# Kernel tuning notes

Hardware: AMD Instinct MI355X
Metric: run time of the kernel (lower is better)

The kernel has to match this reference:

```python
import jax, jax.numpy as jnp
import numpy as np

B, T, C = 4, 2048, 1024
N_HEAD = 16
HEAD_DIM = C // N_HEAD


def setup_inputs() -> dict:
    key = jax.random.key(0)
    k1, k2, k3 = jax.random.split(key, 3)
    x = jax.random.normal(k1, (B, T, C), dtype=jnp.float32)
    w_attn = jax.random.normal(k2, (C, 3 * C), dtype=jnp.float32) * 0.02
    b_attn = jnp.zeros((3 * C,), dtype=jnp.float32)
    # c_proj init stddev = 0.02 / sqrt(2 * n_layer), n_layer = 24
    w_proj = jax.random.normal(k3, (C, C), dtype=jnp.float32) * (0.02 / np.sqrt(48.0))
    b_proj = jnp.zeros((C,), dtype=jnp.float32)
    return {"x": x, "w_attn": w_attn, "b_attn": b_attn,
            "w_proj": w_proj, "b_proj": b_proj}


def reference(x, w_attn, b_attn, w_proj, b_proj):
    Bx, Tx, Cx = x.shape
    scale = 1.0 / jnp.sqrt(jnp.asarray(HEAD_DIM, dtype=x.dtype))
    qkv = x @ w_attn + b_attn                      # [B,T,3C]
    qkv = qkv.reshape(Bx, Tx, 3, N_HEAD, HEAD_DIM)
    q, k, v = qkv[:, :, 0], qkv[:, :, 1], qkv[:, :, 2]  # each [B,T,H,D]
    att = jnp.einsum('bthd,bThd->bhtT', q, k) * scale   # [B,H,T,T]
    mask = jnp.tril(jnp.ones((Tx, Tx), dtype=x.dtype)).reshape(1, 1, Tx, Tx)
    att = att * mask - 1e10 * (1 - mask)
    att = jax.nn.softmax(att, axis=-1)
    y = jnp.einsum('bhtT,bThd->bthd', att, v)      # [B,T,H,D]
    y = y.reshape(Bx, Tx, Cx)
    return y @ w_proj + b_proj
```

## Files before the change

### kernel.cpp

```cpp
#include <hip/hip_runtime.h>
#include <hip/hip_bf16.h>


typedef __attribute__((ext_vector_type(8)))  __bf16 bf16x8;
typedef __attribute__((ext_vector_type(4)))  float  f32x4;
typedef __attribute__((ext_vector_type(16))) float  f32x16;
typedef __attribute__((ext_vector_type(4)))  unsigned int u32x4;

#define AS1C(p) ((const __attribute__((address_space(1))) unsigned int*)(p))
#define AS3(p)  ((__attribute__((address_space(3))) unsigned int*)(p))

__device__ __forceinline__ unsigned short f2bfu(float f){
  __hip_bfloat16 h = __float2bfloat16(f);
  return __builtin_bit_cast(unsigned short, h);
}

__device__ __forceinline__ void plswapu(unsigned int &a, unsigned int &b){
  asm("v_permlane32_swap_b32 %0, %1" : "+v"(a), "+v"(b));
}
__device__ __forceinline__ unsigned int cvtpk(float lo, float hi){
  unsigned int r;
  asm("v_cvt_pk_bf16_f32 %0, %1, %2" : "=v"(r) : "v"(lo), "v"(hi));
  return r;
}
__device__ __forceinline__ float max3f(float a, float b, float c){
  float r;
  asm("v_max3_f32 %0, %1, %2, %3" : "=v"(r) : "v"(a), "v"(b), "v"(c));
  return r;
}


__global__ __launch_bounds__(256)
void f32_to_bf16_vec(const float* __restrict__ in, __hip_bfloat16* __restrict__ out, int n4){
  int stride = gridDim.x * blockDim.x;
  for (int i = blockIdx.x*blockDim.x + threadIdx.x; i < n4; i += stride){
    float4 v = reinterpret_cast<const float4*>(in)[i];
    ushort4 u;
    u.x = f2bfu(v.x); u.y = f2bfu(v.y); u.z = f2bfu(v.z); u.w = f2bfu(v.w);
    reinterpret_cast<ushort4*>(out)[i] = u;
  }
}

__global__ __launch_bounds__(256)
void transpose_to_bf16(const float* __restrict__ in, __hip_bfloat16* __restrict__ out, int R, int C){
  __shared__ float tile[32][33];
  const int tx = threadIdx.x & 31, ty = threadIdx.x >> 5;
  const int c0 = blockIdx.x*32, r0 = blockIdx.y*32;
  for (int i = ty; i < 32; i += 8)
    tile[i][tx] = in[(size_t)(r0+i)*C + c0 + tx];
  __syncthreads();
  for (int i = ty; i < 32; i += 8)
    out[(size_t)(c0+i)*R + r0 + tx] = __float2bfloat16(tile[tx][i]);
}


#define QSCALE 0.1803368801111244f

__device__ __forceinline__ void stage_ab(const __hip_bfloat16* __restrict__ A,
                                         const __hip_bfloat16* __restrict__ Bt,
                                         int m0, int n0, int K, int kt,
                                         __hip_bfloat16* sA, __hip_bfloat16* sB,
                                         int w, int l)
{
  const int k0 = kt*32;
  #pragma unroll
  for (int qq = 0; qq < 2; ++qq){
    const int c = qq*256 + w*64 + l;
    const int row = c>>2, kc = c&3;
    __builtin_amdgcn_global_load_lds(AS1C(A  + (size_t)(m0+row)*K + k0 + 8*kc),
                                     AS3(sA + (qq*256 + w*64)*8), 16, 0, 0);
    __builtin_amdgcn_global_load_lds(AS1C(Bt + (size_t)(n0+row)*K + k0 + 8*kc),
                                     AS3(sB + (qq*256 + w*64)*8), 16, 0, 0);
  }
}

template<int EPI>
__global__ __launch_bounds__(256)
void gemm_bf16(const __hip_bfloat16* __restrict__ A,
               const __hip_bfloat16* __restrict__ Bt,
               const float* __restrict__ bias,
               int M, int N, int K,
               __hip_bfloat16* __restrict__ q_s,
               __hip_bfloat16* __restrict__ k_s,
               __hip_bfloat16* __restrict__ vT_s,
               float* __restrict__ outf)
{
  __shared__ __align__(16) __hip_bfloat16 sA[2][128*32];
  __shared__ __align__(16) __hip_bfloat16 sB[2][128*32];
  const int tid = threadIdx.x, w = tid>>6, l = tid&63, g = l>>4, li = l&15;
  const int wm = w>>1, wn = w&1;

  const int nwg = gridDim.x, cpx = nwg >> 3;
  const int swz = (blockIdx.x & 7)*cpx + (blockIdx.x >> 3);
  const int nbx = N >> 7;
  const int m0 = (swz / nbx)*128, n0 = (swz % nbx)*128;

  f32x4 acc[4][4] = {};

  const int NT = K >> 5;
  stage_ab(A, Bt, m0, n0, K, 0, sA[0], sB[0], w, l);
  int cur = 0;

  for (int kt = 0; kt < NT; ++kt){
    __syncthreads();
    if (kt + 1 < NT)
      stage_ab(A, Bt, m0, n0, K, kt+1, sA[cur^1], sB[cur^1], w, l);

    bf16x8 af[4], bfr[4];
    #pragma unroll
    for (int mi = 0; mi < 4; ++mi)
      af[mi] = *reinterpret_cast<const bf16x8*>(sA[cur] + (wm*64 + mi*16 + li)*32 + 8*g);
    #pragma unroll
    for (int ni = 0; ni < 4; ++ni)
      bfr[ni] = *reinterpret_cast<const bf16x8*>(sB[cur] + (wn*64 + ni*16 + li)*32 + 8*g);
    #pragma unroll
    for (int mi = 0; mi < 4; ++mi)
      #pragma unroll
      for (int ni = 0; ni < 4; ++ni)
        acc[mi][ni] = __builtin_amdgcn_mfma_f32_16x16x32_bf16(af[mi], bfr[ni], acc[mi][ni], 0, 0, 0);
    cur ^= 1;
  }

  #pragma unroll
  for (int ni = 0; ni < 4; ++ni){
    const int col = n0 + wn*64 + ni*16 + li;
    const float bv = bias[col];
    #pragma unroll
    for (int mi = 0; mi < 4; ++mi){
      #pragma unroll
      for (int e = 0; e < 4; ++e){
        const int row = m0 + wm*64 + mi*16 + 4*g + e;
        const float val = acc[mi][ni][e] + bv;
        if (EPI == 0){
          const int three = col >> 10, h = (col >> 6) & 15, d = col & 63;
          const int b = row >> 11, t = row & 2047;
          const int bh = b*16 + h;
          if (three == 0)      q_s[((size_t)bh*2048 + t)*64 + d]  = __float2bfloat16(val*QSCALE);
          else if (three == 1) k_s[((size_t)bh*2048 + t)*64 + d]  = __float2bfloat16(val);
          else                 vT_s[((size_t)bh*64 + d)*2048 + t] = __float2bfloat16(val);
        } else {
          outf[(size_t)row*N + col] = val;
        }
      }
    }
  }
}


__device__ __forceinline__ void stage_kv64(const __hip_bfloat16* __restrict__ k_s,
                                           const __hip_bfloat16* __restrict__ vT_s,
                                           size_t base, int j,
                                           __hip_bfloat16* sk, __hip_bfloat16* svt,
                                           int tid)
{
  #pragma unroll
  for (int it = 0; it < 4; ++it){
    const int c = it*128 + tid;
    const int r = c>>3, cc = c&7;
    __builtin_amdgcn_global_load_lds(AS1C(k_s  + base + (size_t)(j*64 + r)*64 + 8*(cc ^ (r&7))),
                                     AS3(sk  + c*8), 16, 0, 0);
    __builtin_amdgcn_global_load_lds(AS1C(vT_s + base + (size_t)r*2048 + j*64 + 8*(cc ^ (r&7))),
                                     AS3(svt + c*8), 16, 0, 0);
  }
}

__device__ __forceinline__ bf16x8 ldtile(const __hip_bfloat16* t, int row, int chunk){
  return *reinterpret_cast<const bf16x8*>(t + row*64 + ((chunk ^ (row&7))*8));
}

__global__ __launch_bounds__(128, 3)
void flash_attn(const __hip_bfloat16* __restrict__ q_s,
                const __hip_bfloat16* __restrict__ k_s,
                const __hip_bfloat16* __restrict__ vT_s,
                __hip_bfloat16* __restrict__ y_s)
{
  __shared__ __align__(16) __hip_bfloat16 sk [2][64*64];
  __shared__ __align__(16) __hip_bfloat16 svt[2][64*64];

  const int tid = threadIdx.x, w = tid>>6, l = tid&63;
  const int lq = l&31, hf = l>>5, h4 = 4*hf;
  const int bid = blockIdx.x;
  const int xcd = bid & 7, sl = (bid>>3) & 7;
  const int v = 31 - (bid >> 6);
  const int bh = xcd*8 + sl;
  const size_t base = (size_t)bh * (2048*64);
  const int b = bh >> 4, hh = bh & 15;

  const int tw = 2*v + w;
  const int jd = v;
  const int qabs = 32*tw + lq;
  const int rel = 32*w + lq;

  bf16x8 qf[4];
  #pragma unroll
  for (int ks = 0; ks < 4; ++ks)
    qf[ks] = *reinterpret_cast<const bf16x8*>(q_s + base + (size_t)qabs*64 + 16*ks + 8*hf);

  f32x16 o0 = {}, o1 = {};
  float mrun = -1e30f, lrun = 0.f;

  stage_kv64(k_s, vT_s, base, 0, sk[0], svt[0], tid);

  #pragma unroll 1
  for (int j = 0; j <= jd; ++j){
    __syncthreads();
    if (j + 1 <= jd)
      stage_kv64(k_s, vT_s, base, j+1, sk[(j+1)&1], svt[(j+1)&1], tid);

    const __hip_bfloat16* skc  = sk[j&1];
    const __hip_bfloat16* svtc = svt[j&1];

    f32x16 s0 = {}, s1 = {};
    __builtin_amdgcn_s_setprio(1);
    #pragma unroll
    for (int ks = 0; ks < 4; ++ks){
      bf16x8 kf0 = ldtile(skc, lq,      2*ks + hf);
      s0 = __builtin_amdgcn_mfma_f32_32x32x16_bf16(kf0, qf[ks], s0, 0, 0, 0);
      bf16x8 kf1 = ldtile(skc, 32 + lq, 2*ks + hf);
      s1 = __builtin_amdgcn_mfma_f32_32x32x16_bf16(kf1, qf[ks], s1, 0, 0, 0);
    }
    __builtin_amdgcn_s_setprio(0);

    if (j == jd){
      #pragma unroll
      for (int r = 0; r < 16; ++r){
        const int kv0 = (r&3) + 8*(r>>2) + h4;
        s0[r] = (kv0      <= rel) ? s0[r] : -1e30f;
        s1[r] = (kv0 + 32 <= rel) ? s1[r] : -1e30f;
      }
    }

    #define PFX(K) (((K) < 16) ? s0[K] : s1[(K)-16])
    float t0 = max3f(PFX(0),PFX(1),PFX(2)),   t1 = max3f(PFX(3),PFX(4),PFX(5));
    float t2 = max3f(PFX(6),PFX(7),PFX(8)),   t3 = max3f(PFX(9),PFX(10),PFX(11));
    float t4 = max3f(PFX(12),PFX(13),PFX(14)),t5 = max3f(PFX(15),PFX(16),PFX(17));
    float t6 = max3f(PFX(18),PFX(19),PFX(20)),t7 = max3f(PFX(21),PFX(22),PFX(23));
    float t8 = max3f(PFX(24),PFX(25),PFX(26)),t9 = max3f(PFX(27),PFX(28),PFX(29));
    float t10 = fmaxf(PFX(30),PFX(31));
    float u0 = max3f(t0,t1,t2), u1 = max3f(t3,t4,t5), u2 = max3f(t6,t7,t8);
    float u3 = fmaxf(t9,t10);
    float pm = fmaxf(max3f(u0,u1,u2), u3);
    #undef PFX

    if (!__all(pm - mrun <= 8.0f)){
      pm = fmaxf(pm, __shfl_xor(pm, 32));
      const float nm = fmaxf(mrun, pm);
      const float corr = exp2f(mrun - nm);
      mrun = nm;
      o0 *= corr; o1 *= corr;
      lrun *= corr;
    }

    #pragma unroll
    for (int r = 0; r < 16; ++r){
      s0[r] = exp2f(s0[r] - mrun);
      s1[r] = exp2f(s1[r] - mrun);
    }

    float c16[16];
    #pragma unroll
    for (int k = 0; k < 16; ++k) c16[k] = s0[k] + s1[k];
    float d8[8];
    #pragma unroll
    for (int k = 0; k < 8; ++k) d8[k] = c16[k] + c16[k+8];
    float d4a = d8[0]+d8[4], d4b = d8[1]+d8[5], d4c = d8[2]+d8[6], d4d = d8[3]+d8[7];
    float psum = (d4a+d4c) + (d4b+d4d);
    psum += __shfl_xor(psum, 32);
    lrun += psum;

    unsigned int wds[16];
    #pragma unroll
    for (int k = 0; k < 8; ++k) wds[k]   = cvtpk(s0[2*k], s0[2*k+1]);
    #pragma unroll
    for (int k = 0; k < 8; ++k) wds[8+k] = cvtpk(s1[2*k], s1[2*k+1]);
    #pragma unroll
    for (int a = 0; a < 2; ++a)
      #pragma unroll
      for (int bl = 0; bl < 2; ++bl){
        plswapu(wds[a*8 + 4*bl    ], wds[a*8 + 4*bl + 2]);
        plswapu(wds[a*8 + 4*bl + 1], wds[a*8 + 4*bl + 3]);
      }
    bf16x8 pfr[4];
    #pragma unroll
    for (int B = 0; B < 4; ++B){
      u32x4 tt = { wds[4*B], wds[4*B+1], wds[4*B+2], wds[4*B+3] };
      pfr[B] = __builtin_bit_cast(bf16x8, tt);
    }

    __builtin_amdgcn_s_setprio(1);
    #pragma unroll
    for (int ks = 0; ks < 4; ++ks){
      bf16x8 vf0 = ldtile(svtc, lq,      2*ks + hf);
      o0 = __builtin_amdgcn_mfma_f32_32x32x16_bf16(vf0, pfr[ks], o0, 0, 0, 0);
      bf16x8 vf1 = ldtile(svtc, 32 + lq, 2*ks + hf);
      o1 = __builtin_amdgcn_mfma_f32_32x32x16_bf16(vf1, pfr[ks], o1, 0, 0, 0);
    }
    __builtin_amdgcn_s_setprio(0);
  }

  const float inv = 1.f / lrun;
  __hip_bfloat16* yp = y_s + ((size_t)(b*2048 + qabs))*1024 + hh*64;
  #pragma unroll
  for (int i = 0; i < 8; ++i){
    const int d = (2*i & 3) + 8*(i>>1) + h4;
    *reinterpret_cast<unsigned int*>(yp + d)      = cvtpk(o0[2*i]*inv, o0[2*i+1]*inv);
    *reinterpret_cast<unsigned int*>(yp + 32 + d) = cvtpk(o1[2*i]*inv, o1[2*i+1]*inv);
  }
}


extern "C" void kernel_launch(void* const* d_in, const int* in_sizes, int n_in,
                              void* d_out, int out_size, void* d_ws, size_t ws_size,
                              hipStream_t stream)
{
  const float* x      = (const float*)d_in[0];
  const float* w_attn = (const float*)d_in[1];
  const float* b_attn = (const float*)d_in[2];
  const float* w_proj = (const float*)d_in[3];
  const float* b_proj = (const float*)d_in[4];
  float* out = (float*)d_out;
  char* ws = (char*)d_ws;

  __hip_bfloat16* xb     = (__hip_bfloat16*)(ws + 0);
  __hip_bfloat16* wattnT = (__hip_bfloat16*)(ws + 16777216);
  __hip_bfloat16* wprojT = (__hip_bfloat16*)(ws + 23068672);
  __hip_bfloat16* q_s    = (__hip_bfloat16*)(ws + 25165824);
  __hip_bfloat16* k_s    = (__hip_bfloat16*)(ws + 41943040);
  __hip_bfloat16* vT_s   = (__hip_bfloat16*)(ws + 58720256);
  __hip_bfloat16* y_s    = xb;

  f32_to_bf16_vec<<<2048, 256, 0, stream>>>(x, xb, 8388608/4);
  transpose_to_bf16<<<dim3(3072/32, 1024/32), 256, 0, stream>>>(w_attn, wattnT, 1024, 3072);
  transpose_to_bf16<<<dim3(1024/32, 1024/32), 256, 0, stream>>>(w_proj, wprojT, 1024, 1024);

  gemm_bf16<0><<<1536, 256, 0, stream>>>(
      xb, wattnT, b_attn, 8192, 3072, 1024, q_s, k_s, vT_s, (float*)nullptr);

  flash_attn<<<2048, 128, 0, stream>>>(q_s, k_s, vT_s, y_s);

  gemm_bf16<1><<<512, 256, 0, stream>>>(
      y_s, wprojT, b_proj, 8192, 1024, 1024,
      (__hip_bfloat16*)nullptr, (__hip_bfloat16*)nullptr, (__hip_bfloat16*)nullptr, out);
}
```

Baseline: 212.4 us.

## Widen flash-attention blocks to 8 waves sharing one K/V stream

Each flash-attention block now runs 512 threads covering 256 query rows instead of 128 threads covering 64, so one staged K/V tile is shared by 8 waves rather than 2. Each thread issues a single load per tensor per tile, and waves whose causal range has ended skip compute but still take part in the barriers. Block ordering is remapped to a middle-out group schedule for load balance. The intended gain is less redundant K/V traffic to LDS and fewer, larger blocks; the cost is idle waves on the diagonal tiles and coarser scheduling with only 512 blocks.

```diff
diff --git a/kernel.cpp b/kernel.cpp
--- a/kernel.cpp
+++ b/kernel.cpp
@@ -147,28 +147,24 @@
 }
 
 
-__device__ __forceinline__ void stage_kv64(const __hip_bfloat16* __restrict__ k_s,
-                                           const __hip_bfloat16* __restrict__ vT_s,
-                                           size_t base, int j,
-                                           __hip_bfloat16* sk, __hip_bfloat16* svt,
-                                           int tid)
-{
-  #pragma unroll
-  for (int it = 0; it < 4; ++it){
-    const int c = it*128 + tid;
-    const int r = c>>3, cc = c&7;
-    __builtin_amdgcn_global_load_lds(AS1C(k_s  + base + (size_t)(j*64 + r)*64 + 8*(cc ^ (r&7))),
-                                     AS3(sk  + c*8), 16, 0, 0);
-    __builtin_amdgcn_global_load_lds(AS1C(vT_s + base + (size_t)r*2048 + j*64 + 8*(cc ^ (r&7))),
-                                     AS3(svt + c*8), 16, 0, 0);
-  }
+__device__ __forceinline__ void stage_kv512(const __hip_bfloat16* __restrict__ k_s,
+                                            const __hip_bfloat16* __restrict__ vT_s,
+                                            size_t base, int j,
+                                            __hip_bfloat16* sk, __hip_bfloat16* svt,
+                                            int tid)
+{
+  const int r = tid>>3, cc = tid&7;
+  __builtin_amdgcn_global_load_lds(AS1C(k_s  + base + (size_t)(j*64 + r)*64 + 8*(cc ^ (r&7))),
+                                   AS3(sk  + tid*8), 16, 0, 0);
+  __builtin_amdgcn_global_load_lds(AS1C(vT_s + base + (size_t)r*2048 + j*64 + 8*(cc ^ (r&7))),
+                                   AS3(svt + tid*8), 16, 0, 0);
 }
 
 __device__ __forceinline__ bf16x8 ldtile(const __hip_bfloat16* t, int row, int chunk){
   return *reinterpret_cast<const bf16x8*>(t + row*64 + ((chunk ^ (row&7))*8));
 }
 
-__global__ __launch_bounds__(128, 3)
+__global__ __launch_bounds__(512, 4)
 void flash_attn(const __hip_bfloat16* __restrict__ q_s,
                 const __hip_bfloat16* __restrict__ k_s,
                 const __hip_bfloat16* __restrict__ vT_s,
@@ -181,15 +177,16 @@
   const int lq = l&31, hf = l>>5, h4 = 4*hf;
   const int bid = blockIdx.x;
   const int xcd = bid & 7, sl = (bid>>3) & 7;
-  const int v = 31 - (bid >> 6);
+  const int gr = bid >> 6;
+  const int g = (gr < 4) ? (7 - gr) : (gr - 4);
   const int bh = xcd*8 + sl;
   const size_t base = (size_t)bh * (2048*64);
   const int b = bh >> 4, hh = bh & 15;
 
-  const int tw = 2*v + w;
-  const int jd = v;
-  const int qabs = 32*tw + lq;
-  const int rel = 32*w + lq;
+  const int jdw  = 4*g + (w >> 1);
+  const int jmax = 4*g + 3;
+  const int rel  = 32*(w & 1) + lq;
+  const int qabs = 256*g + 32*w + lq;
 
   bf16x8 qf[4];
   #pragma unroll
@@ -199,103 +196,105 @@
   f32x16 o0 = {}, o1 = {};
   float mrun = -1e30f, lrun = 0.f;
 
-  stage_kv64(k_s, vT_s, base, 0, sk[0], svt[0], tid);
+  stage_kv512(k_s, vT_s, base, 0, sk[0], svt[0], tid);
 
   #pragma unroll 1
-  for (int j = 0; j <= jd; ++j){
+  for (int j = 0; j <= jmax; ++j){
     __syncthreads();
-    if (j + 1 <= jd)
-      stage_kv64(k_s, vT_s, base, j+1, sk[(j+1)&1], svt[(j+1)&1], tid);
-
-    const __hip_bfloat16* skc  = sk[j&1];
-    const __hip_bfloat16* svtc = svt[j&1];
-
-    f32x16 s0 = {}, s1 = {};
-    __builtin_amdgcn_s_setprio(1);
-    #pragma unroll
-    for (int ks = 0; ks < 4; ++ks){
-      bf16x8 kf0 = ldtile(skc, lq,      2*ks + hf);
-      s0 = __builtin_amdgcn_mfma_f32_32x32x16_bf16(kf0, qf[ks], s0, 0, 0, 0);
-      bf16x8 kf1 = ldtile(skc, 32 + lq, 2*ks + hf);
-      s1 = __builtin_amdgcn_mfma_f32_32x32x16_bf16(kf1, qf[ks], s1, 0, 0, 0);
+    if (j + 1 <= jmax)
+      stage_kv512(k_s, vT_s, base, j+1, sk[(j+1)&1], svt[(j+1)&1], tid);
+
+    if (j <= jdw){
+      const __hip_bfloat16* skc  = sk[j&1];
+      const __hip_bfloat16* svtc = svt[j&1];
+
+      f32x16 s0 = {}, s1 = {};
+      __builtin_amdgcn_s_setprio(1);
+      #pragma unroll
+      for (int ks = 0; ks < 4; ++ks){
+        bf16x8 kf0 = ldtile(skc, lq,      2*ks + hf);
+        s0 = __builtin_amdgcn_mfma_f32_32x32x16_bf16(kf0, qf[ks], s0, 0, 0, 0);
+        bf16x8 kf1 = ldtile(skc, 32 + lq, 2*ks + hf);
+        s1 = __builtin_amdgcn_mfma_f32_32x32x16_bf16(kf1, qf[ks], s1, 0, 0, 0);
+      }
+      __builtin_amdgcn_s_setprio(0);
+
+      if (j == jdw){
+        #pragma unroll
+        for (int r = 0; r < 16; ++r){
+          const int kv0 = (r&3) + 8*(r>>2) + h4;
+          s0[r] = (kv0      <= rel) ? s0[r] : -1e30f;
+          s1[r] = (kv0 + 32 <= rel) ? s1[r] : -1e30f;
+        }
+      }
+
+      #define PFX(K) (((K) < 16) ? s0[K] : s1[(K)-16])
+      float t0 = max3f(PFX(0),PFX(1),PFX(2)),   t1 = max3f(PFX(3),PFX(4),PFX(5));
+      float t2 = max3f(PFX(6),PFX(7),PFX(8)),   t3 = max3f(PFX(9),PFX(10),PFX(11));
+      float t4 = max3f(PFX(12),PFX(13),PFX(14)),t5 = max3f(PFX(15),PFX(16),PFX(17));
+      float t6 = max3f(PFX(18),PFX(19),PFX(20)),t7 = max3f(PFX(21),PFX(22),PFX(23));
+      float t8 = max3f(PFX(24),PFX(25),PFX(26)),t9 = max3f(PFX(27),PFX(28),PFX(29));
+      float t10 = fmaxf(PFX(30),PFX(31));
+      float u0 = max3f(t0,t1,t2), u1 = max3f(t3,t4,t5), u2 = max3f(t6,t7,t8);
+      float u3 = fmaxf(t9,t10);
+      float pm = fmaxf(max3f(u0,u1,u2), u3);
+      #undef PFX
+
+      if (!__all(pm - mrun <= 8.0f)){
+        pm = fmaxf(pm, __shfl_xor(pm, 32));
+        const float nm = fmaxf(mrun, pm);
+        const float corr = exp2f(mrun - nm);
+        mrun = nm;
+        o0 *= corr; o1 *= corr;
+        lrun *= corr;
+      }
+
+      #pragma unroll
+      for (int r = 0; r < 16; ++r){
+        s0[r] = exp2f(s0[r] - mrun);
+        s1[r] = exp2f(s1[r] - mrun);
+      }
+
+      float c16[16];
+      #pragma unroll
+      for (int k = 0; k < 16; ++k) c16[k] = s0[k] + s1[k];
+      float d8[8];
+      #pragma unroll
+      for (int k = 0; k < 8; ++k) d8[k] = c16[k] + c16[k+8];
+      float d4a = d8[0]+d8[4], d4b = d8[1]+d8[5], d4c = d8[2]+d8[6], d4d = d8[3]+d8[7];
+      float psum = (d4a+d4c) + (d4b+d4d);
+      psum += __shfl_xor(psum, 32);
+      lrun += psum;
+
+      unsigned int wds[16];
+      #pragma unroll
+      for (int k = 0; k < 8; ++k) wds[k]   = cvtpk(s0[2*k], s0[2*k+1]);
+      #pragma unroll
+      for (int k = 0; k < 8; ++k) wds[8+k] = cvtpk(s1[2*k], s1[2*k+1]);
+      #pragma unroll
+      for (int a = 0; a < 2; ++a)
+        #pragma unroll
+        for (int bl = 0; bl < 2; ++bl){
+          plswapu(wds[a*8 + 4*bl    ], wds[a*8 + 4*bl + 2]);
+          plswapu(wds[a*8 + 4*bl + 1], wds[a*8 + 4*bl + 3]);
+        }
+      bf16x8 pfr[4];
+      #pragma unroll
+      for (int B = 0; B < 4; ++B){
+        u32x4 tt = { wds[4*B], wds[4*B+1], wds[4*B+2], wds[4*B+3] };
+        pfr[B] = __builtin_bit_cast(bf16x8, tt);
+      }
+
+      __builtin_amdgcn_s_setprio(1);
+      #pragma unroll
+      for (int ks = 0; ks < 4; ++ks){
+        bf16x8 vf0 = ldtile(svtc, lq,      2*ks + hf);
+        o0 = __builtin_amdgcn_mfma_f32_32x32x16_bf16(vf0, pfr[ks], o0, 0, 0, 0);
+        bf16x8 vf1 = ldtile(svtc, 32 + lq, 2*ks + hf);
+        o1 = __builtin_amdgcn_mfma_f32_32x32x16_bf16(vf1, pfr[ks], o1, 0, 0, 0);
+      }
+      __builtin_amdgcn_s_setprio(0);
     }
-    __builtin_amdgcn_s_setprio(0);
-
-    if (j == jd){
-      #pragma unroll
-      for (int r = 0; r < 16; ++r){
-        const int kv0 = (r&3) + 8*(r>>2) + h4;
-        s0[r] = (kv0      <= rel) ? s0[r] : -1e30f;
-        s1[r] = (kv0 + 32 <= rel) ? s1[r] : -1e30f;
-      }
-    }
-
-    #define PFX(K) (((K) < 16) ? s0[K] : s1[(K)-16])
-    float t0 = max3f(PFX(0),PFX(1),PFX(2)),   t1 = max3f(PFX(3),PFX(4),PFX(5));
-    float t2 = max3f(PFX(6),PFX(7),PFX(8)),   t3 = max3f(PFX(9),PFX(10),PFX(11));
-    float t4 = max3f(PFX(12),PFX(13),PFX(14)),t5 = max3f(PFX(15),PFX(16),PFX(17));
-    float t6 = max3f(PFX(18),PFX(19),PFX(20)),t7 = max3f(PFX(21),PFX(22),PFX(23));
-    float t8 = max3f(PFX(24),PFX(25),PFX(26)),t9 = max3f(PFX(27),PFX(28),PFX(29));
-    float t10 = fmaxf(PFX(30),PFX(31));
-    float u0 = max3f(t0,t1,t2), u1 = max3f(t3,t4,t5), u2 = max3f(t6,t7,t8);
-    float u3 = fmaxf(t9,t10);
-    float pm = fmaxf(max3f(u0,u1,u2), u3);
-    #undef PFX
-
-    if (!__all(pm - mrun <= 8.0f)){
-      pm = fmaxf(pm, __shfl_xor(pm, 32));
-      const float nm = fmaxf(mrun, pm);
-      const float corr = exp2f(mrun - nm);
-      mrun = nm;
-      o0 *= corr; o1 *= corr;
-      lrun *= corr;
-    }
-
-    #pragma unroll
-    for (int r = 0; r < 16; ++r){
-      s0[r] = exp2f(s0[r] - mrun);
-      s1[r] = exp2f(s1[r] - mrun);
-    }
-
-    float c16[16];
-    #pragma unroll
-    for (int k = 0; k < 16; ++k) c16[k] = s0[k] + s1[k];
-    float d8[8];
-    #pragma unroll
-    for (int k = 0; k < 8; ++k) d8[k] = c16[k] + c16[k+8];
-    float d4a = d8[0]+d8[4], d4b = d8[1]+d8[5], d4c = d8[2]+d8[6], d4d = d8[3]+d8[7];
-    float psum = (d4a+d4c) + (d4b+d4d);
-    psum += __shfl_xor(psum, 32);
-    lrun += psum;
-
-    unsigned int wds[16];
-    #pragma unroll
-    for (int k = 0; k < 8; ++k) wds[k]   = cvtpk(s0[2*k], s0[2*k+1]);
-    #pragma unroll
-    for (int k = 0; k < 8; ++k) wds[8+k] = cvtpk(s1[2*k], s1[2*k+1]);
-    #pragma unroll
-    for (int a = 0; a < 2; ++a)
-      #pragma unroll
-      for (int bl = 0; bl < 2; ++bl){
-        plswapu(wds[a*8 + 4*bl    ], wds[a*8 + 4*bl + 2]);
-        plswapu(wds[a*8 + 4*bl + 1], wds[a*8 + 4*bl + 3]);
-      }
-    bf16x8 pfr[4];
-    #pragma unroll
-    for (int B = 0; B < 4; ++B){
-      u32x4 tt = { wds[4*B], wds[4*B+1], wds[4*B+2], wds[4*B+3] };
-      pfr[B] = __builtin_bit_cast(bf16x8, tt);
-    }
-
-    __builtin_amdgcn_s_setprio(1);
-    #pragma unroll
-    for (int ks = 0; ks < 4; ++ks){
-      bf16x8 vf0 = ldtile(svtc, lq,      2*ks + hf);
-      o0 = __builtin_amdgcn_mfma_f32_32x32x16_bf16(vf0, pfr[ks], o0, 0, 0, 0);
-      bf16x8 vf1 = ldtile(svtc, 32 + lq, 2*ks + hf);
-      o1 = __builtin_amdgcn_mfma_f32_32x32x16_bf16(vf1, pfr[ks], o1, 0, 0, 0);
-    }
-    __builtin_amdgcn_s_setprio(0);
   }
 
   const float inv = 1.f / lrun;
@@ -336,7 +335,7 @@
   gemm_bf16<0><<<1536, 256, 0, stream>>>(
       xb, wattnT, b_attn, 8192, 3072, 1024, q_s, k_s, vT_s, (float*)nullptr);
 
-  flash_attn<<<2048, 128, 0, stream>>>(q_s, k_s, vT_s, y_s);
+  flash_attn<<<512, 512, 0, stream>>>(q_s, k_s, vT_s, y_s);
 
   gemm_bf16<1><<<512, 256, 0, stream>>>(
       y_s, wprojT, b_proj, 8192, 1024, 1024,
```

New measurement: 224.9 us. 1.06x slower.
